# Performance work log

Hardware: AMD Instinct MI355X
Metric: run time of the kernel (lower is better)

Reference implementation:

```python
import jax, jax.numpy as jnp
import numpy as np

TAU_MIN, TAU_MAX, TAU_SMALL, N_REF = 0.005, 0.1, 0.3, 4


def _l2norm(x, eps=1e-12):
    # matches torch F.normalize: x / max(||x||_2, eps)
    n = jnp.linalg.norm(x, axis=-1, keepdims=True)
    return x / jnp.maximum(n, eps)


def setup_inputs() -> dict:
    key = jax.random.key(0)
    k1, k2, k3 = jax.random.split(key, 3)
    B, C, H, W = 8, 384, 40, 40
    feats = jax.random.normal(k1, (B, C, H, W), dtype=jnp.float32)
    refs = jax.random.normal(k2, (N_REF, B, C, H, W), dtype=jnp.float32)
    sopm = jax.random.uniform(k3, (B, 1, 160, 160), dtype=jnp.float32)
    log_tau = jnp.array([np.log(0.03)], dtype=jnp.float32)
    alpha_raw = jnp.array([0.0], dtype=jnp.float32)
    return {"feats": feats, "refs": refs, "sopm": sopm,
            "log_tau": log_tau, "alpha_raw": alpha_raw}


def reference(feats, refs, sopm, log_tau, alpha_raw):
    B, C, H, W = feats.shape
    N = H * W
    # buffer contents and SOPM cache are detached in the torch module
    refs = jax.lax.stop_gradient(refs)
    sopm = jax.lax.stop_gradient(sopm)

    tau = jnp.clip(jnp.exp(log_tau[0]), TAU_MIN, TAU_MAX)
    alpha = jax.nn.sigmoid(alpha_raw[0])

    tokens = feats.reshape(B, C, N).transpose(0, 2, 1)   # [B, N, C]
    cur_n = _l2norm(tokens)

    n_ref = refs.shape[0]
    warped_sum = jnp.zeros_like(tokens)
    for r in range(n_ref):  # fixed small ref-frame loop (n_ref=4)
        ref_tok = refs[r].reshape(B, C, N).transpose(0, 2, 1)  # [B, N, C]
        ref_n = _l2norm(ref_tok)
        sim = jnp.einsum('bnc,bmc->bnm', cur_n, ref_n)          # cosine sims
        w = jax.nn.softmax(sim / tau, axis=-1)                  # [B, N, N]
        warped_sum = warped_sum + jnp.einsum('bnm,bmc->bnc', w, ref_tok)
    warped = warped_sum / n_ref

    # SOPM(t-1) -> bilinear resize (align_corners=False) -> threshold mask
    sopm_r = jax.image.resize(sopm, (B, 1, H, W), method='bilinear')
    mask = (sopm_r.reshape(B, 1, N).transpose(0, 2, 1) > TAU_SMALL).astype(feats.dtype)  # [B,N,1]

    alpha_eff = alpha  # full buffer: n_avail == n_ref
    fused = alpha_eff * warped + (1.0 - alpha_eff) * tokens
    enhanced = mask * fused + (1.0 - mask) * tokens
    return enhanced.transpose(0, 2, 1).reshape(B, C, H, W)
```

## Files before the change

### kernel.cpp

```cpp
#include <hip/hip_runtime.h>
#include <stdint.h>

#define B_  8
#define C_  384
#define N_  1600
#define R_  4
#define S_  160
#define HW_ 40

typedef float  f32x4  __attribute__((ext_vector_type(4)));
typedef __bf16 bf16x8 __attribute__((ext_vector_type(8)));
typedef long long i64t;

__device__ __forceinline__ unsigned short f2bf(float x){
  __bf16 h = (__bf16)x;
  return __builtin_bit_cast(unsigned short, h);
}
__device__ __forceinline__ float bf2f(unsigned short u){
  return __builtin_bit_cast(float, (uint32_t)u << 16);
}
__device__ __forceinline__ uint32_t pk_fp8x4(float a, float b, float c, float d){
  int lo = __builtin_amdgcn_cvt_pk_fp8_f32(a, b, 0, false);
  int hi = __builtin_amdgcn_cvt_pk_fp8_f32(c, d, 0, false);
  return (uint32_t)(lo & 0xffff) | ((uint32_t)hi << 16);
}

__device__ __forceinline__ void gload_lds16(const void* g, void* l){
  __builtin_amdgcn_global_load_lds(
      (const __attribute__((address_space(1))) uint32_t*)g,
      (__attribute__((address_space(3))) uint32_t*)l, 16, 0, 0);
}

__global__ void norm_kernel(const float* __restrict__ feats,
                            const float* __restrict__ refs,
                            float* __restrict__ invn){
  int gid = blockIdx.x * 256 + threadIdx.x;
  if (gid >= 16000) return;
  int mat = gid / 400;
  int n4  = (gid - mat * 400) * 4;
  const float* src = (mat < B_) ? (feats + (size_t)mat * C_ * N_)
                                : (refs  + (size_t)(mat - B_) * C_ * N_);
  f32x4 ss = {0.f,0.f,0.f,0.f};
  for (int c = 0; c < C_; ++c){
    f32x4 v = *(const f32x4*)(src + (size_t)c * N_ + n4);
    ss += v * v;
  }
  f32x4 r;
#pragma unroll
  for (int i = 0; i < 4; ++i) r[i] = 1.f / fmaxf(sqrtf(ss[i]), 1e-12f);
  *(f32x4*)(invn + (size_t)mat * N_ + n4) = r;
}

__global__ void prep_kernel(const float* __restrict__ feats,
                            const float* __restrict__ refs,
                            const float* __restrict__ invn,
                            unsigned char* __restrict__ Qb,
                            unsigned char* __restrict__ Kb,
                            unsigned short* __restrict__ Vb){
  int nt = blockIdx.x, ct = blockIdx.y, mat = blockIdx.z;
  __shared__ float tile[64][65];
  int t = threadIdx.x;
  bool isref = (mat >= B_);
  const float* src = isref ? refs  + (size_t)(mat - B_) * C_ * N_
                           : feats + (size_t)mat * C_ * N_;
#pragma unroll
  for (int i = 0; i < 4; ++i){
    int chunk = t + 256 * i;
    int cr = chunk >> 4, n4 = chunk & 15;
    size_t off = (size_t)(ct * 64 + cr) * N_ + nt * 64 + n4 * 4;
    float4 v = *(const float4*)(src + off);
    tile[cr][n4 * 4 + 0] = v.x;  tile[cr][n4 * 4 + 1] = v.y;
    tile[cr][n4 * 4 + 2] = v.z;  tile[cr][n4 * 4 + 3] = v.w;
    if (isref){
      ushort4 o;
      o.x = f2bf(v.x); o.y = f2bf(v.y); o.z = f2bf(v.z); o.w = f2bf(v.w);
      unsigned short* vdst = Vb + (size_t)(mat - B_) * C_ * N_;
      *(ushort4*)(vdst + off) = o;
    }
  }
  __syncthreads();
  unsigned char* dst = isref ? Kb + (size_t)(mat - B_) * N_ * C_
                             : Qb + (size_t)mat * N_ * C_;
  const float* ivp = invn + (size_t)mat * N_ + nt * 64;
#pragma unroll
  for (int i = 0; i < 4; ++i){
    int chunk = t + 256 * i;
    int nr = chunk >> 4, c4 = chunk & 15;
    float iv = ivp[nr];
    uint32_t pk = pk_fp8x4(tile[c4*4+0][nr] * iv, tile[c4*4+1][nr] * iv,
                           tile[c4*4+2][nr] * iv, tile[c4*4+3][nr] * iv);
    *(uint32_t*)(dst + (size_t)(nt*64+nr) * C_ + ct*64 + c4*4) = pk;
  }
}

__global__ void mask_kernel(const float* __restrict__ sopm,
                            float* __restrict__ maskp){
  int gid = blockIdx.x * 256 + threadIdx.x;
  int b = gid / N_, n = gid - b * N_;
  int oy = n / HW_, ox = n - oy * HW_;
  const float* sp = sopm + (size_t)b * S_ * S_;
  float cy = oy * 4 + 1.5f, cx = ox * 4 + 1.5f;
  int y0 = 4*oy - 2; if (y0 < 0) y0 = 0;
  int y1 = 4*oy + 5; if (y1 > S_-1) y1 = S_-1;
  int x0 = 4*ox - 2; if (x0 < 0) x0 = 0;
  int x1 = 4*ox + 5; if (x1 > S_-1) x1 = S_-1;
  float wsy = 0.f, wsx = 0.f;
  for (int j = y0; j <= y1; ++j) wsy += 1.f - fabsf(j - cy) * 0.25f;
  for (int j = x0; j <= x1; ++j) wsx += 1.f - fabsf(j - cx) * 0.25f;
  float acc = 0.f;
  for (int jy = y0; jy <= y1; ++jy){
    float wy = 1.f - fabsf(jy - cy) * 0.25f;
    float rs = 0.f;
    for (int jx = x0; jx <= x1; ++jx)
      rs += (1.f - fabsf(jx - cx) * 0.25f) * sp[jy * S_ + jx];
    acc += wy * rs;
  }
  float val = acc / (wsy * wsx);
  maskp[gid] = (val > 0.3f) ? 1.f : 0.f;
}

#define V_OFF  12288
#define P_OFF  36864
#define LDS_SZ 40960

__global__ __launch_bounds__(256, 2) void attn_kernel(
    const unsigned char* __restrict__ Qb,
    const unsigned char* __restrict__ Kb,
    const unsigned short* __restrict__ Vb,
    const float* __restrict__ log_tau,
    unsigned short* __restrict__ Or)
{
  __shared__ __align__(16) char lds[LDS_SZ];
  int wg   = blockIdx.x;
  int orig = (wg & 7) * 100 + (wg >> 3);
  int qt   = orig % 25;
  int rb   = orig / 25;
  int b    = rb & 7;
  int tid  = threadIdx.x;
  int lane = tid & 63;
  int w    = tid >> 6;
  int l15  = lane & 15;
  int lg   = lane >> 4;

  float tau = expf(log_tau[0]);
  tau = fminf(fmaxf(tau, 0.005f), 0.1f);
  float sc = 1.4426950408889634f / tau;

  i64t qf[12];
  int qrow = qt * 64 + w * 16 + l15;
  const unsigned char* qp = Qb + ((size_t)b * N_ + qrow) * C_ + lg * 8;
#pragma unroll
  for (int ks = 0; ks < 12; ++ks)
    qf[ks] = *(const i64t*)(qp + ks * 32);

  f32x4 o[4][6];
#pragma unroll
  for (int i = 0; i < 4; ++i)
#pragma unroll
    for (int j = 0; j < 6; ++j) o[i][j] = (f32x4){0.f,0.f,0.f,0.f};
  float lsum = 0.f;

  const unsigned char*  kmat = Kb + (size_t)rb * N_ * C_;
  const unsigned short* vmat = Vb + (size_t)rb * C_ * N_;
  char* Pb = lds + P_OFF;

  int koffB[3], voff[6];
#pragma unroll
  for (int i = 0; i < 3; ++i){
    int L = (w * 3 + i) * 64 + lane;
    int m   = L / 24;
    int pos = L - m * 24;
    int cc  = (pos >> 3) * 8 + ((pos & 7) ^ (m & 7));
    koffB[i] = m * C_ + cc * 16;
  }
#pragma unroll
  for (int i = 0; i < 6; ++i){
    int chunk = (w * 6 + i) * 64 + lane;
    int line = chunk >> 3;
    int u    = (chunk & 7) ^ (line & 7);
    voff[i]  = (line * 2 + (u >> 2)) * N_ + (u & 3) * 8;
  }
  char* kdst = lds + (size_t)(w * 3) * 1024;
  char* vdst = lds + V_OFF + (size_t)(w * 6) * 1024;

  const int s_l  = (l15 >> 1) & 3;
  const int p_w0 = (w*16 + l15) * 64 + (((lg >> 1)       ^ s_l) << 4) + (lg & 1) * 8;
  const int p_w1 = (w*16 + l15) * 64 + ((((lg >> 1) + 2) ^ s_l) << 4) + (lg & 1) * 8;
  const int p_rc = ((lg ^ s_l) << 4) + l15 * 64;

  auto stageK = [&](int t){
    const unsigned char* kb = kmat + (size_t)t * 32 * C_;
#pragma unroll
    for (int i = 0; i < 3; ++i) gload_lds16(kb + koffB[i], kdst + i * 1024);
  };
  auto stageV = [&](int t){
    const unsigned short* vb = vmat + t * 32;
#pragma unroll
    for (int i = 0; i < 6; ++i) gload_lds16(vb + voff[i], vdst + i * 1024);
  };

  stageK(0);
  stageV(0);
  asm volatile("s_waitcnt vmcnt(6)" ::: "memory");
  __builtin_amdgcn_sched_barrier(0);
  __builtin_amdgcn_s_barrier();
  __builtin_amdgcn_sched_barrier(0);

  for (int mt = 0; mt < 50; ++mt){
    f32x4 s0 = {0.f,0.f,0.f,0.f}, s1 = {0.f,0.f,0.f,0.f};
    __builtin_amdgcn_s_setprio(1);
#pragma unroll
    for (int ks = 0; ks < 12; ++ks){
      int lc  = 2 * ks + (lg >> 1);
      int off = ((lc >> 3) * 8 + ((lc & 7) ^ (l15 & 7))) * 16 + (lg & 1) * 8;
      i64t a0 = *(const i64t*)(lds + l15 * 384 + off);
      i64t a1 = *(const i64t*)(lds + (l15 + 16) * 384 + off);
      s0 = __builtin_amdgcn_mfma_f32_16x16x32_fp8_fp8(a0, qf[ks], s0, 0, 0, 0);
      s1 = __builtin_amdgcn_mfma_f32_16x16x32_fp8_fp8(a1, qf[ks], s1, 0, 0, 0);
    }
    __builtin_amdgcn_s_setprio(0);

    asm volatile("s_waitcnt vmcnt(0)" ::: "memory");
    __builtin_amdgcn_sched_barrier(0);
    __builtin_amdgcn_s_barrier();
    __builtin_amdgcn_sched_barrier(0);
    if (mt < 49) stageK(mt + 1);

    ushort4 pw0, pw1;
    float ls = 0.f;
    {
      __bf16 h;
      h = (__bf16)exp2f((s0[0]-1.f)*sc); ls += (float)h; pw0.x = __builtin_bit_cast(unsigned short, h);
      h = (__bf16)exp2f((s0[1]-1.f)*sc); ls += (float)h; pw0.y = __builtin_bit_cast(unsigned short, h);
      h = (__bf16)exp2f((s0[2]-1.f)*sc); ls += (float)h; pw0.z = __builtin_bit_cast(unsigned short, h);
      h = (__bf16)exp2f((s0[3]-1.f)*sc); ls += (float)h; pw0.w = __builtin_bit_cast(unsigned short, h);
      h = (__bf16)exp2f((s1[0]-1.f)*sc); ls += (float)h; pw1.x = __builtin_bit_cast(unsigned short, h);
      h = (__bf16)exp2f((s1[1]-1.f)*sc); ls += (float)h; pw1.y = __builtin_bit_cast(unsigned short, h);
      h = (__bf16)exp2f((s1[2]-1.f)*sc); ls += (float)h; pw1.z = __builtin_bit_cast(unsigned short, h);
      h = (__bf16)exp2f((s1[3]-1.f)*sc); ls += (float)h; pw1.w = __builtin_bit_cast(unsigned short, h);
    }
    lsum += ls;
    *(ushort4*)(Pb + p_w0) = pw0;
    *(ushort4*)(Pb + p_w1) = pw1;
    asm volatile("s_waitcnt lgkmcnt(0)" ::: "memory");
    __builtin_amdgcn_sched_barrier(0);
    __builtin_amdgcn_s_barrier();
    __builtin_amdgcn_sched_barrier(0);

    bf16x8 pa[4];
#pragma unroll
    for (int qf2 = 0; qf2 < 4; ++qf2)
      pa[qf2] = *(const bf16x8*)(Pb + qf2 * 1024 + p_rc);
    __builtin_amdgcn_s_setprio(1);
#pragma unroll
    for (int cf = 0; cf < 6; ++cf){
      int c  = w * 96 + cf * 16 + l15;
      int vo = V_OFF + (c >> 1) * 128 + (((lg | ((c & 1) << 2)) ^ ((c >> 1) & 7)) << 4);
      bf16x8 vf = *(const bf16x8*)(lds + vo);
#pragma unroll
      for (int qf2 = 0; qf2 < 4; ++qf2)
        o[qf2][cf] = __builtin_amdgcn_mfma_f32_16x16x32_bf16(pa[qf2], vf, o[qf2][cf], 0, 0, 0);
    }
    __builtin_amdgcn_s_setprio(0);

    __builtin_amdgcn_sched_barrier(0);
    __builtin_amdgcn_s_barrier();
    __builtin_amdgcn_sched_barrier(0);
    if (mt < 49) stageV(mt + 1);
    asm volatile("s_waitcnt vmcnt(6)" ::: "memory");
    __builtin_amdgcn_sched_barrier(0);
    __builtin_amdgcn_s_barrier();
    __builtin_amdgcn_sched_barrier(0);
  }

  lsum += __shfl_xor(lsum, 16, 64);
  lsum += __shfl_xor(lsum, 32, 64);
  __syncthreads();
  float* lsh = (float*)(lds + P_OFF);
  if (lg == 0) lsh[w * 16 + l15] = lsum;
  __syncthreads();
  float invl[4][4];
#pragma unroll
  for (int qf2 = 0; qf2 < 4; ++qf2)
#pragma unroll
    for (int rg = 0; rg < 4; ++rg)
      invl[qf2][rg] = 1.f / lsh[qf2 * 16 + lg * 4 + rg];

  int qbase = qt * 64;
  unsigned short* op = Or + ((size_t)rb * N_ + qbase) * C_ + w * 96 + l15;
#pragma unroll
  for (int qf2 = 0; qf2 < 4; ++qf2){
#pragma unroll
    for (int cf = 0; cf < 6; ++cf){
#pragma unroll
      for (int rg = 0; rg < 4; ++rg){
        int q = qf2 * 16 + lg * 4 + rg;
        op[(size_t)q * C_ + cf * 16] = f2bf(o[qf2][cf][rg] * invl[qf2][rg]);
      }
    }
  }
}

__global__ void combine_kernel(const unsigned short* __restrict__ Or,
                               const float* __restrict__ feats,
                               const float* __restrict__ maskp,
                               const float* __restrict__ alpha_raw,
                               float* __restrict__ out){
  int nt = blockIdx.x, ct = blockIdx.y, b = blockIdx.z;
  __shared__ float tile[64][65];
  float alpha = 1.f / (1.f + expf(-alpha_raw[0]));
  int t = threadIdx.x;
#pragma unroll
  for (int i = 0; i < 4; ++i){
    int chunk = t + 256 * i;
    int nr = chunk >> 4, c4 = chunk & 15;
    size_t base = ((size_t)b * N_ + nt * 64 + nr) * C_ + ct * 64 + c4 * 4;
    float4 s = {0.f,0.f,0.f,0.f};
#pragma unroll
    for (int r = 0; r < 4; ++r){
      ushort4 v = *(const ushort4*)(Or + (size_t)r * B_ * N_ * C_ + base);
      s.x += bf2f(v.x); s.y += bf2f(v.y); s.z += bf2f(v.z); s.w += bf2f(v.w);
    }
    tile[nr][c4*4+0] = s.x; tile[nr][c4*4+1] = s.y;
    tile[nr][c4*4+2] = s.z; tile[nr][c4*4+3] = s.w;
  }
  __syncthreads();
#pragma unroll
  for (int i = 0; i < 4; ++i){
    int chunk = t + 256 * i;
    int cr = chunk >> 4, n4 = chunk & 15;
    size_t fb = ((size_t)b * C_ + ct * 64 + cr) * N_ + nt * 64 + n4 * 4;
    float4 f  = *(const float4*)(feats + fb);
    float4 mk = *(const float4*)(maskp + (size_t)b * N_ + nt * 64 + n4 * 4);
    float4 ov;
    ov.x = f.x + mk.x * alpha * (tile[n4*4+0][cr] * 0.25f - f.x);
    ov.y = f.y + mk.y * alpha * (tile[n4*4+1][cr] * 0.25f - f.y);
    ov.z = f.z + mk.z * alpha * (tile[n4*4+2][cr] * 0.25f - f.z);
    ov.w = f.w + mk.w * alpha * (tile[n4*4+3][cr] * 0.25f - f.w);
    *(float4*)(out + fb) = ov;
  }
}

__global__ void poison_kernel(float* out, int n){
  int i = blockIdx.x * 256 + threadIdx.x;
  if (i < n) out[i] = 1.0e6f;
}

extern "C" void kernel_launch(void* const* d_in, const int* in_sizes, int n_in,
                              void* d_out, int out_size, void* d_ws, size_t ws_size,
                              hipStream_t stream){
  const float* feats     = (const float*)d_in[0];
  const float* refs      = (const float*)d_in[1];
  const float* sopm      = (const float*)d_in[2];
  const float* log_tau   = (const float*)d_in[3];
  const float* alpha_raw = (const float*)d_in[4];
  float* out = (float*)d_out;

  const size_t SZ_INVN = (size_t)(1 + R_) * B_ * N_ * 4;
  const size_t SZ_MASK = (size_t)B_ * N_ * 4;
  const size_t SZ_QB   = (size_t)B_ * N_ * C_;
  const size_t SZ_KB   = (size_t)R_ * B_ * N_ * C_;
  const size_t SZ_VB   = (size_t)R_ * B_ * N_ * C_ * 2;
  const size_t SZ_OR   = (size_t)R_ * B_ * N_ * C_ * 2;
  const size_t need = SZ_INVN + SZ_MASK + SZ_QB + SZ_KB + SZ_VB + SZ_OR;

  if (ws_size < need){
    poison_kernel<<<(out_size + 255) / 256, 256, 0, stream>>>(out, out_size);
    return;
  }
  char* ws = (char*)d_ws;
  float*          invn  = (float*)ws;
  float*          maskp = (float*)(ws + SZ_INVN);
  unsigned char*  Qb    = (unsigned char*)(ws + SZ_INVN + SZ_MASK);
  unsigned char*  Kb    = (unsigned char*)(ws + SZ_INVN + SZ_MASK + SZ_QB);
  unsigned short* Vb    = (unsigned short*)(ws + SZ_INVN + SZ_MASK + SZ_QB + SZ_KB);
  unsigned short* Or    = (unsigned short*)(ws + SZ_INVN + SZ_MASK + SZ_QB + SZ_KB + SZ_VB);

  norm_kernel   <<<63, 256, 0, stream>>>(feats, refs, invn);
  mask_kernel   <<<50, 256, 0, stream>>>(sopm, maskp);
  prep_kernel   <<<dim3(25, 6, 40), 256, 0, stream>>>(feats, refs, invn, Qb, Kb, Vb);
  attn_kernel   <<<800, 256, 0, stream>>>(Qb, Kb, Vb, log_tau, Or);
  combine_kernel<<<dim3(25, 6, 8), 256, 0, stream>>>(Or, feats, maskp, alpha_raw, out);
}
```

Measured before the change: 242.5 us.

## Load V fragments directly from global into registers and repartition QK work across waves

V tiles are no longer staged through LDS. Each wave now reads its bf16 V fragments straight from global memory into registers at the top of each key tile, which cuts the LDS footprint from 40 KB to 16 KB and removes one barrier per iteration. The QK^T step is repartitioned so each wave handles 16 key rows against two 32-query sub-blocks, sharing one K fragment across two MFMAs. Row sums are then combined across wave pairs through LDS. The risk is that global V load latency sits on the critical path, and the loads are per-lane 16-byte strided reads that may coalesce less well.

```diff
diff --git a/kernel.cpp b/kernel.cpp
--- a/kernel.cpp
+++ b/kernel.cpp
@@ -119,9 +119,8 @@
   maskp[gid] = (val > 0.3f) ? 1.f : 0.f;
 }
 
-#define V_OFF  12288
-#define P_OFF  36864
-#define LDS_SZ 40960
+#define P_OFF  12288
+#define LDS_SZ 16384
 
 __global__ __launch_bounds__(256, 2) void attn_kernel(
     const unsigned char* __restrict__ Qb,
@@ -139,6 +138,8 @@
   int tid  = threadIdx.x;
   int lane = tid & 63;
   int w    = tid >> 6;
+  int mw   = w >> 1;
+  int qw   = w & 1;
   int l15  = lane & 15;
   int lg   = lane >> 4;
 
@@ -146,25 +147,28 @@
   tau = fminf(fmaxf(tau, 0.005f), 0.1f);
   float sc = 1.4426950408889634f / tau;
 
-  i64t qf[12];
-  int qrow = qt * 64 + w * 16 + l15;
-  const unsigned char* qp = Qb + ((size_t)b * N_ + qrow) * C_ + lg * 8;
-#pragma unroll
-  for (int ks = 0; ks < 12; ++ks)
-    qf[ks] = *(const i64t*)(qp + ks * 32);
+  i64t qreg[2][12];
+#pragma unroll
+  for (int qt2 = 0; qt2 < 2; ++qt2){
+    const unsigned char* qp = Qb +
+        ((size_t)b * N_ + qt * 64 + qw * 32 + qt2 * 16 + l15) * C_ + lg * 8;
+#pragma unroll
+    for (int ks = 0; ks < 12; ++ks)
+      qreg[qt2][ks] = *(const i64t*)(qp + ks * 32);
+  }
 
   f32x4 o[4][6];
 #pragma unroll
   for (int i = 0; i < 4; ++i)
 #pragma unroll
     for (int j = 0; j < 6; ++j) o[i][j] = (f32x4){0.f,0.f,0.f,0.f};
-  float lsum = 0.f;
+  float lsum0 = 0.f, lsum1 = 0.f;
 
   const unsigned char*  kmat = Kb + (size_t)rb * N_ * C_;
   const unsigned short* vmat = Vb + (size_t)rb * C_ * N_;
   char* Pb = lds + P_OFF;
 
-  int koffB[3], voff[6];
+  int koffB[3];
 #pragma unroll
   for (int i = 0; i < 3; ++i){
     int L = (w * 3 + i) * 64 + lane;
@@ -173,19 +177,16 @@
     int cc  = (pos >> 3) * 8 + ((pos & 7) ^ (m & 7));
     koffB[i] = m * C_ + cc * 16;
   }
-#pragma unroll
-  for (int i = 0; i < 6; ++i){
-    int chunk = (w * 6 + i) * 64 + lane;
-    int line = chunk >> 3;
-    int u    = (chunk & 7) ^ (line & 7);
-    voff[i]  = (line * 2 + (u >> 2)) * N_ + (u & 3) * 8;
-  }
   char* kdst = lds + (size_t)(w * 3) * 1024;
-  char* vdst = lds + V_OFF + (size_t)(w * 6) * 1024;
+
+  const unsigned short* vptr[6];
+#pragma unroll
+  for (int cf = 0; cf < 6; ++cf)
+    vptr[cf] = vmat + (size_t)(w * 96 + cf * 16 + l15) * N_ + lg * 8;
 
   const int s_l  = (l15 >> 1) & 3;
-  const int p_w0 = (w*16 + l15) * 64 + (((lg >> 1)       ^ s_l) << 4) + (lg & 1) * 8;
-  const int p_w1 = (w*16 + l15) * 64 + ((((lg >> 1) + 2) ^ s_l) << 4) + (lg & 1) * 8;
+  const int p_w0 = (qw*32      + l15) * 64 + (((2*mw + (lg >> 1)) ^ s_l) << 4) + (lg & 1) * 8;
+  const int p_w1 = (qw*32 + 16 + l15) * 64 + (((2*mw + (lg >> 1)) ^ s_l) << 4) + (lg & 1) * 8;
   const int p_rc = ((lg ^ s_l) << 4) + l15 * 64;
 
   auto stageK = [&](int t){
@@ -193,53 +194,54 @@
 #pragma unroll
     for (int i = 0; i < 3; ++i) gload_lds16(kb + koffB[i], kdst + i * 1024);
   };
-  auto stageV = [&](int t){
-    const unsigned short* vb = vmat + t * 32;
-#pragma unroll
-    for (int i = 0; i < 6; ++i) gload_lds16(vb + voff[i], vdst + i * 1024);
-  };
 
   stageK(0);
-  stageV(0);
-  asm volatile("s_waitcnt vmcnt(6)" ::: "memory");
+  asm volatile("s_waitcnt vmcnt(0)" ::: "memory");
   __builtin_amdgcn_sched_barrier(0);
   __builtin_amdgcn_s_barrier();
   __builtin_amdgcn_sched_barrier(0);
 
+  const int krow = (mw * 16 + l15);
   for (int mt = 0; mt < 50; ++mt){
+    bf16x8 vf[6];
+#pragma unroll
+    for (int cf = 0; cf < 6; ++cf){
+      vf[cf] = *(const bf16x8*)(vptr[cf]);
+      vptr[cf] += 32;
+    }
+    __builtin_amdgcn_sched_barrier(0);
+
     f32x4 s0 = {0.f,0.f,0.f,0.f}, s1 = {0.f,0.f,0.f,0.f};
     __builtin_amdgcn_s_setprio(1);
 #pragma unroll
     for (int ks = 0; ks < 12; ++ks){
       int lc  = 2 * ks + (lg >> 1);
-      int off = ((lc >> 3) * 8 + ((lc & 7) ^ (l15 & 7))) * 16 + (lg & 1) * 8;
-      i64t a0 = *(const i64t*)(lds + l15 * 384 + off);
-      i64t a1 = *(const i64t*)(lds + (l15 + 16) * 384 + off);
-      s0 = __builtin_amdgcn_mfma_f32_16x16x32_fp8_fp8(a0, qf[ks], s0, 0, 0, 0);
-      s1 = __builtin_amdgcn_mfma_f32_16x16x32_fp8_fp8(a1, qf[ks], s1, 0, 0, 0);
+      int off = ((lc >> 3) * 8 + ((lc & 7) ^ (krow & 7))) * 16 + (lg & 1) * 8;
+      i64t a = *(const i64t*)(lds + krow * 384 + off);
+      s0 = __builtin_amdgcn_mfma_f32_16x16x32_fp8_fp8(a, qreg[0][ks], s0, 0, 0, 0);
+      s1 = __builtin_amdgcn_mfma_f32_16x16x32_fp8_fp8(a, qreg[1][ks], s1, 0, 0, 0);
     }
     __builtin_amdgcn_s_setprio(0);
 
-    asm volatile("s_waitcnt vmcnt(0)" ::: "memory");
     __builtin_amdgcn_sched_barrier(0);
     __builtin_amdgcn_s_barrier();
     __builtin_amdgcn_sched_barrier(0);
     if (mt < 49) stageK(mt + 1);
 
     ushort4 pw0, pw1;
-    float ls = 0.f;
     {
       __bf16 h;
-      h = (__bf16)exp2f((s0[0]-1.f)*sc); ls += (float)h; pw0.x = __builtin_bit_cast(unsigned short, h);
-      h = (__bf16)exp2f((s0[1]-1.f)*sc); ls += (float)h; pw0.y = __builtin_bit_cast(unsigned short, h);
-      h = (__bf16)exp2f((s0[2]-1.f)*sc); ls += (float)h; pw0.z = __builtin_bit_cast(unsigned short, h);
-      h = (__bf16)exp2f((s0[3]-1.f)*sc); ls += (float)h; pw0.w = __builtin_bit_cast(unsigned short, h);
-      h = (__bf16)exp2f((s1[0]-1.f)*sc); ls += (float)h; pw1.x = __builtin_bit_cast(unsigned short, h);
-      h = (__bf16)exp2f((s1[1]-1.f)*sc); ls += (float)h; pw1.y = __builtin_bit_cast(unsigned short, h);
-      h = (__bf16)exp2f((s1[2]-1.f)*sc); ls += (float)h; pw1.z = __builtin_bit_cast(unsigned short, h);
-      h = (__bf16)exp2f((s1[3]-1.f)*sc); ls += (float)h; pw1.w = __builtin_bit_cast(unsigned short, h);
-    }
-    lsum += ls;
+      float l0 = 0.f, l1 = 0.f;
+      h = (__bf16)exp2f((s0[0]-1.f)*sc); l0 += (float)h; pw0.x = __builtin_bit_cast(unsigned short, h);
+      h = (__bf16)exp2f((s0[1]-1.f)*sc); l0 += (float)h; pw0.y = __builtin_bit_cast(unsigned short, h);
+      h = (__bf16)exp2f((s0[2]-1.f)*sc); l0 += (float)h; pw0.z = __builtin_bit_cast(unsigned short, h);
+      h = (__bf16)exp2f((s0[3]-1.f)*sc); l0 += (float)h; pw0.w = __builtin_bit_cast(unsigned short, h);
+      h = (__bf16)exp2f((s1[0]-1.f)*sc); l1 += (float)h; pw1.x = __builtin_bit_cast(unsigned short, h);
+      h = (__bf16)exp2f((s1[1]-1.f)*sc); l1 += (float)h; pw1.y = __builtin_bit_cast(unsigned short, h);
+      h = (__bf16)exp2f((s1[2]-1.f)*sc); l1 += (float)h; pw1.z = __builtin_bit_cast(unsigned short, h);
+      h = (__bf16)exp2f((s1[3]-1.f)*sc); l1 += (float)h; pw1.w = __builtin_bit_cast(unsigned short, h);
+      lsum0 += l0; lsum1 += l1;
+    }
     *(ushort4*)(Pb + p_w0) = pw0;
     *(ushort4*)(Pb + p_w1) = pw1;
     asm volatile("s_waitcnt lgkmcnt(0)" ::: "memory");
@@ -254,37 +256,37 @@
     __builtin_amdgcn_s_setprio(1);
 #pragma unroll
     for (int cf = 0; cf < 6; ++cf){
-      int c  = w * 96 + cf * 16 + l15;
-      int vo = V_OFF + (c >> 1) * 128 + (((lg | ((c & 1) << 2)) ^ ((c >> 1) & 7)) << 4);
-      bf16x8 vf = *(const bf16x8*)(lds + vo);
 #pragma unroll
       for (int qf2 = 0; qf2 < 4; ++qf2)
-        o[qf2][cf] = __builtin_amdgcn_mfma_f32_16x16x32_bf16(pa[qf2], vf, o[qf2][cf], 0, 0, 0);
+        o[qf2][cf] = __builtin_amdgcn_mfma_f32_16x16x32_bf16(pa[qf2], vf[cf], o[qf2][cf], 0, 0, 0);
     }
     __builtin_amdgcn_s_setprio(0);
 
+    asm volatile("s_waitcnt vmcnt(0)" ::: "memory");
     __builtin_amdgcn_sched_barrier(0);
     __builtin_amdgcn_s_barrier();
     __builtin_amdgcn_sched_barrier(0);
-    if (mt < 49) stageV(mt + 1);
-    asm volatile("s_waitcnt vmcnt(6)" ::: "memory");
-    __builtin_amdgcn_sched_barrier(0);
-    __builtin_amdgcn_s_barrier();
-    __builtin_amdgcn_sched_barrier(0);
-  }
-
-  lsum += __shfl_xor(lsum, 16, 64);
-  lsum += __shfl_xor(lsum, 32, 64);
+  }
+
+  lsum0 += __shfl_xor(lsum0, 16, 64);
+  lsum0 += __shfl_xor(lsum0, 32, 64);
+  lsum1 += __shfl_xor(lsum1, 16, 64);
+  lsum1 += __shfl_xor(lsum1, 32, 64);
   __syncthreads();
-  float* lsh = (float*)(lds + P_OFF);
-  if (lg == 0) lsh[w * 16 + l15] = lsum;
+  float* lsh = (float*)lds;
+  if (lg == 0){
+    lsh[mw * 64 + qw * 32 + l15]      = lsum0;
+    lsh[mw * 64 + qw * 32 + 16 + l15] = lsum1;
+  }
   __syncthreads();
   float invl[4][4];
 #pragma unroll
   for (int qf2 = 0; qf2 < 4; ++qf2)
 #pragma unroll
-    for (int rg = 0; rg < 4; ++rg)
-      invl[qf2][rg] = 1.f / lsh[qf2 * 16 + lg * 4 + rg];
+    for (int rg = 0; rg < 4; ++rg){
+      int q = qf2 * 16 + lg * 4 + rg;
+      invl[qf2][rg] = 1.f / (lsh[q] + lsh[64 + q]);
+    }
 
   int qbase = qt * 64;
   unsigned short* op = Or + ((size_t)rb * N_ + qbase) * C_ + w * 96 + l15;
```

Measured after the change: 276.0 us. 1.14x slower.
